# Optimization experiments

Measured on AMD Instinct MI355X. Metric: run time of the kernel, lower is better.

## Reference

```python
import jax, jax.numpy as jnp
import numpy as np

B, S, IN_F, OUT_F, GROUP = 2, 1024, 4096, 4096, 128
N_GROUPS = IN_F // GROUP  # 32


def setup_inputs() -> dict:
    key = jax.random.key(0)
    k1, k2, k3, k4 = jax.random.split(key, 4)
    x = jax.random.normal(k1, (B, S, IN_F), dtype=jnp.float32)
    # int4-range weights stored in int8, symmetric quant in [-7, 7]
    w_q = jax.random.randint(k2, (OUT_F, N_GROUPS, GROUP), -7, 8, dtype=jnp.int8)
    # per-(group, out_feature) scales, positive
    s_w = jax.random.uniform(k3, (N_GROUPS, OUT_F), dtype=jnp.float32,
                             minval=1e-3, maxval=2e-2)
    bias = jax.random.normal(k4, (OUT_F,), dtype=jnp.float32)
    return {"x": x, "w_q": w_q, "s_w": s_w, "bias": bias}


def reference(x, w_q, s_w, bias):
    # Faithful to QuantLinearW4Grouped.forward:
    #   y_g = einsum('ngk,ogk->ngo', x_f, w_f); y = (y_g * s_w[None]).sum(1) + bias
    # Expressed as a single fused einsum (identical math, no (n,g,o) intermediate).
    prefix = x.shape[:-1]
    orig_dtype = x.dtype
    xg = x.reshape(-1, N_GROUPS, GROUP).astype(jnp.float32)  # (n, g, k)
    w_f = w_q.astype(jnp.float32)                            # (o, g, k)
    y = jnp.einsum('ngk,ogk,go->no', xg, w_f, s_w)           # (n, o)
    y = y + bias.astype(y.dtype)
    return y.reshape(*prefix, OUT_F).astype(orig_dtype)
```

## Files before the change

### kernel.cpp

```cpp
#include <hip/hip_runtime.h>
#include <hip/hip_bf16.h>
#include <stdint.h>

#define M_TOK 2048
#define N_OUT 4096
#define K_IN  4096
#define GROUPSZ 128
#define NGRP  32

typedef signed char i8;
typedef int    intx4  __attribute__((ext_vector_type(4)));
typedef float  floatx4 __attribute__((ext_vector_type(4)));

#define XQ_BLOCKS (M_TOK)
#define WQ_BLOCKS (N_OUT * K_IN / 16 / 256)

__global__ __launch_bounds__(256) void quant_kernel(
    const float* __restrict__ x, const int* __restrict__ wq,
    i8* __restrict__ xq, i8* __restrict__ wq8, float* __restrict__ sx) {
  __shared__ float red[4];
  int b = blockIdx.x;
  int tid = threadIdx.x;
  if (b < XQ_BLOCKS) {
    const float* xr = x + (size_t)b * K_IN;
    int e0 = tid * 16;
    float4 v0 = *(const float4*)(xr + e0);
    float4 v1 = *(const float4*)(xr + e0 + 4);
    float4 v2 = *(const float4*)(xr + e0 + 8);
    float4 v3 = *(const float4*)(xr + e0 + 12);
    float m = fabsf(v0.x);
    m = fmaxf(m, fabsf(v0.y)); m = fmaxf(m, fabsf(v0.z)); m = fmaxf(m, fabsf(v0.w));
    m = fmaxf(m, fabsf(v1.x)); m = fmaxf(m, fabsf(v1.y)); m = fmaxf(m, fabsf(v1.z)); m = fmaxf(m, fabsf(v1.w));
    m = fmaxf(m, fabsf(v2.x)); m = fmaxf(m, fabsf(v2.y)); m = fmaxf(m, fabsf(v2.z)); m = fmaxf(m, fabsf(v2.w));
    m = fmaxf(m, fabsf(v3.x)); m = fmaxf(m, fabsf(v3.y)); m = fmaxf(m, fabsf(v3.z)); m = fmaxf(m, fabsf(v3.w));
#pragma unroll
    for (int off = 32; off > 0; off >>= 1)
      m = fmaxf(m, __shfl_xor(m, off, 64));
    int lane = tid & 63, wv = tid >> 6;
    if (lane == 0) red[wv] = m;
    __syncthreads();
    m = fmaxf(fmaxf(red[0], red[1]), fmaxf(red[2], red[3]));
    float inv = (m > 0.f) ? 127.f / m : 0.f;
    union { i8 q[16]; int4 v; } u;
    u.q[0]  = (i8)(int)rintf(v0.x * inv); u.q[1]  = (i8)(int)rintf(v0.y * inv);
    u.q[2]  = (i8)(int)rintf(v0.z * inv); u.q[3]  = (i8)(int)rintf(v0.w * inv);
    u.q[4]  = (i8)(int)rintf(v1.x * inv); u.q[5]  = (i8)(int)rintf(v1.y * inv);
    u.q[6]  = (i8)(int)rintf(v1.z * inv); u.q[7]  = (i8)(int)rintf(v1.w * inv);
    u.q[8]  = (i8)(int)rintf(v2.x * inv); u.q[9]  = (i8)(int)rintf(v2.y * inv);
    u.q[10] = (i8)(int)rintf(v2.z * inv); u.q[11] = (i8)(int)rintf(v2.w * inv);
    u.q[12] = (i8)(int)rintf(v3.x * inv); u.q[13] = (i8)(int)rintf(v3.y * inv);
    u.q[14] = (i8)(int)rintf(v3.z * inv); u.q[15] = (i8)(int)rintf(v3.w * inv);
    *(int4*)(xq + (size_t)b * K_IN + e0) = u.v;
    if (tid == 0) sx[b] = m * (1.f / 127.f);
  } else {
    size_t t = (size_t)(b - XQ_BLOCKS) * 256 + tid;
    size_t base = t * 16;
    const int* src = wq + base;
    int4 a0 = *(const int4*)(src);
    int4 a1 = *(const int4*)(src + 4);
    int4 a2 = *(const int4*)(src + 8);
    int4 a3 = *(const int4*)(src + 12);
    union { i8 q[16]; int4 v; } u;
    u.q[0]  = (i8)a0.x; u.q[1]  = (i8)a0.y; u.q[2]  = (i8)a0.z; u.q[3]  = (i8)a0.w;
    u.q[4]  = (i8)a1.x; u.q[5]  = (i8)a1.y; u.q[6]  = (i8)a1.z; u.q[7]  = (i8)a1.w;
    u.q[8]  = (i8)a2.x; u.q[9]  = (i8)a2.y; u.q[10] = (i8)a2.z; u.q[11] = (i8)a2.w;
    u.q[12] = (i8)a3.x; u.q[13] = (i8)a3.y; u.q[14] = (i8)a3.z; u.q[15] = (i8)a3.w;
    *(int4*)(wq8 + base) = u.v;
  }
}

#define BM 128
#define BN 128
#define BK 128

__global__ __launch_bounds__(256, 2) void gemm_i8_kernel(
    const i8* __restrict__ Aq, const i8* __restrict__ Bq,
    const float* __restrict__ sx, const float* __restrict__ sw,
    const float* __restrict__ bias, float* __restrict__ C) {
  __shared__ i8 As[BM * BK];
  __shared__ i8 Bs[BN * BK];
  __shared__ float sws[NGRP * BN];
  __shared__ float sxs[BM];

  const int tid  = threadIdx.x;
  const int lane = tid & 63;
  const int wave = tid >> 6;
  const int bm = blockIdx.y;
  const int bn = blockIdx.x;
  const int wm = wave >> 1;
  const int wn = wave & 1;

  const int rowA0 = bm * BM;
  const int rowB0 = bn * BN;

  {
    int g = tid >> 3, c0 = (tid & 7) * 16;
    const float* src = sw + (size_t)g * N_OUT + rowB0 + c0;
    float* dst = sws + g * BN + c0;
    *(float4*)(dst)      = *(const float4*)(src);
    *(float4*)(dst + 4)  = *(const float4*)(src + 4);
    *(float4*)(dst + 8)  = *(const float4*)(src + 8);
    *(float4*)(dst + 12) = *(const float4*)(src + 12);
    if (tid < BM) sxs[tid] = sx[rowA0 + tid];
  }

  const i8* srcA[4]; const i8* srcB[4];
#pragma unroll
  for (int i = 0; i < 4; ++i) {
    int chunk = i * 256 + tid;
    int row = chunk >> 3;
    int col = ((chunk & 7) ^ (row & 7)) << 4;
    srcA[i] = Aq + (size_t)(rowA0 + row) * K_IN + col;
    srcB[i] = Bq + (size_t)(rowB0 + row) * K_IN + col;
  }

  floatx4 master[4][4];
#pragma unroll
  for (int i = 0; i < 4; ++i)
#pragma unroll
    for (int j = 0; j < 4; ++j) master[i][j] = (floatx4)0.0f;

  const int quad = lane >> 4;
  const int l16  = lane & 15;
  const int h    = l16 & 7;
  const int x0   = (quad ^ h) * 16;
  const int x1   = x0 ^ 64;

  const intx4 MAGICV = {0x4B400000, 0x4B400000, 0x4B400000, 0x4B400000};
  const float MAGICF = 12582912.0f;

  for (int k0 = 0, g = 0; k0 < K_IN; k0 += BK, ++g) {
    __syncthreads();
#pragma unroll
    for (int i = 0; i < 4; ++i) {
      __builtin_amdgcn_global_load_lds(
          (const __attribute__((address_space(1))) void*)(srcA[i] + k0),
          (__attribute__((address_space(3))) void*)(As + (size_t)(i * 256 + wave * 64) * 16),
          16, 0, 0);
      __builtin_amdgcn_global_load_lds(
          (const __attribute__((address_space(1))) void*)(srcB[i] + k0),
          (__attribute__((address_space(3))) void*)(Bs + (size_t)(i * 256 + wave * 64) * 16),
          16, 0, 0);
    }
    __syncthreads();

    float swv[4];
#pragma unroll
    for (int j = 0; j < 4; ++j)
      swv[j] = sws[g * BN + wn * 64 + j * 16 + l16];

    intx4 a0[4], a1[4], b0[4], b1[4];
#pragma unroll
    for (int i = 0; i < 4; ++i) {
      const i8* pa = As + (size_t)(wm * 64 + i * 16 + l16) * BK;
      a0[i] = *(const intx4*)(pa + x0);
      a1[i] = *(const intx4*)(pa + x1);
    }
#pragma unroll
    for (int j = 0; j < 4; ++j) {
      const i8* pb = Bs + (size_t)(wn * 64 + j * 16 + l16) * BK;
      b0[j] = *(const intx4*)(pb + x0);
      b1[j] = *(const intx4*)(pb + x1);
    }

#pragma unroll
    for (int i = 0; i < 4; ++i)
#pragma unroll
      for (int j = 0; j < 4; ++j) {
        intx4 acc = __builtin_amdgcn_mfma_i32_16x16x64_i8(a0[i], b0[j], MAGICV, 0, 0, 0);
        acc = __builtin_amdgcn_mfma_i32_16x16x64_i8(a1[i], b1[j], acc, 0, 0, 0);
        floatx4 t = __builtin_bit_cast(floatx4, acc) - MAGICF;
        master[i][j] += t * swv[j];
      }
  }

#pragma unroll
  for (int j = 0; j < 4; ++j) {
    int col = rowB0 + wn * 64 + j * 16 + l16;
    float bv = bias[col];
#pragma unroll
    for (int i = 0; i < 4; ++i) {
      int rloc = wm * 64 + i * 16 + quad * 4;
#pragma unroll
      for (int r = 0; r < 4; ++r) {
        C[(size_t)(rowA0 + rloc + r) * N_OUT + col] =
            master[i][j][r] * sxs[rloc + r] + bv;
      }
    }
  }
}

extern "C" void kernel_launch(void* const* d_in, const int* in_sizes, int n_in,
                              void* d_out, int out_size, void* d_ws, size_t ws_size,
                              hipStream_t stream) {
  const float* x    = (const float*)d_in[0];
  const int*   wq   = (const int*)d_in[1];
  const float* sw   = (const float*)d_in[2];
  const float* bias = (const float*)d_in[3];
  float* out = (float*)d_out;

  i8*    xq  = (i8*)d_ws;
  i8*    wq8 = (i8*)((char*)d_ws + (size_t)M_TOK * K_IN);
  float* sx  = (float*)((char*)d_ws + (size_t)M_TOK * K_IN
                                     + (size_t)N_OUT * K_IN);

  {
    int nblocks = XQ_BLOCKS + WQ_BLOCKS;
    quant_kernel<<<nblocks, 256, 0, stream>>>(x, wq, xq, wq8, sx);
  }
  {
    dim3 grid(N_OUT / BN, M_TOK / BM);
    gemm_i8_kernel<<<grid, 256, 0, stream>>>(xq, wq8, sx, sw, bias, out);
  }
}
```

Measured before the change: 173.3 us.

## Double-buffer GEMM LDS tiles with 512-thread blocks and BK=64 prefetch pipeline

```diff
diff --git a/kernel.cpp b/kernel.cpp
--- a/kernel.cpp
+++ b/kernel.cpp
@@ -11,6 +11,9 @@
 typedef signed char i8;
 typedef int    intx4  __attribute__((ext_vector_type(4)));
 typedef float  floatx4 __attribute__((ext_vector_type(4)));
+
+#define AS1 __attribute__((address_space(1)))
+#define AS3 __attribute__((address_space(3)))
 
 #define XQ_BLOCKS (M_TOK)
 #define WQ_BLOCKS (N_OUT * K_IN / 16 / 256)
@@ -69,22 +72,24 @@
   }
 }
 
-#define BM 128
+#define BM 256
 #define BN 128
-#define BK 128
-
-__global__ __launch_bounds__(256, 2) void gemm_i8_kernel(
+#define BK 64
+#define NT (K_IN / BK)
+
+__global__ __launch_bounds__(512, 2) void gemm_i8_kernel(
     const i8* __restrict__ Aq, const i8* __restrict__ Bq,
     const float* __restrict__ sx, const float* __restrict__ sw,
     const float* __restrict__ bias, float* __restrict__ C) {
-  __shared__ i8 As[BM * BK];
-  __shared__ i8 Bs[BN * BK];
+  __shared__ i8 As[2 * BM * BK];
+  __shared__ i8 Bs[2 * BN * BK];
   __shared__ float sws[NGRP * BN];
-  __shared__ float sxs[BM];
 
   const int tid  = threadIdx.x;
   const int lane = tid & 63;
   const int wave = tid >> 6;
+  const int quad = lane >> 4;
+  const int l16  = lane & 15;
   const int bm = blockIdx.y;
   const int bn = blockIdx.x;
   const int wm = wave >> 1;
@@ -93,99 +98,101 @@
   const int rowA0 = bm * BM;
   const int rowB0 = bn * BN;
 
+  const int cA0 = tid, cA1 = 512 + tid, cB = tid;
+  const i8* srcA0 = Aq + (size_t)(rowA0 + (cA0 >> 2)) * K_IN
+                       + (((cA0 & 3) ^ ((cA0 >> 2) & 3)) << 4);
+  const i8* srcA1 = Aq + (size_t)(rowA0 + (cA1 >> 2)) * K_IN
+                       + (((cA1 & 3) ^ ((cA1 >> 2) & 3)) << 4);
+  const i8* srcB0 = Bq + (size_t)(rowB0 + (cB >> 2)) * K_IN
+                       + (((cB & 3) ^ ((cB >> 2) & 3)) << 4);
+  i8* dstA0 = As + (size_t)(wave * 64) * 16;
+  i8* dstA1 = As + (size_t)(512 + wave * 64) * 16;
+  i8* dstB0 = Bs + (size_t)(wave * 64) * 16;
+
+  auto stage = [&](int buf, int t) {
+    const size_t ko = (size_t)t * BK;
+    __builtin_amdgcn_global_load_lds(
+        (const AS1 void*)(srcA0 + ko),
+        (AS3 void*)(dstA0 + (size_t)buf * (BM * BK)), 16, 0, 0);
+    __builtin_amdgcn_global_load_lds(
+        (const AS1 void*)(srcA1 + ko),
+        (AS3 void*)(dstA1 + (size_t)buf * (BM * BK)), 16, 0, 0);
+    __builtin_amdgcn_global_load_lds(
+        (const AS1 void*)(srcB0 + ko),
+        (AS3 void*)(dstB0 + (size_t)buf * (BN * BK)), 16, 0, 0);
+  };
+
+  stage(0, 0);
   {
-    int g = tid >> 3, c0 = (tid & 7) * 16;
+    int g = tid >> 4, c0 = (tid & 15) * 8;
     const float* src = sw + (size_t)g * N_OUT + rowB0 + c0;
     float* dst = sws + g * BN + c0;
-    *(float4*)(dst)      = *(const float4*)(src);
-    *(float4*)(dst + 4)  = *(const float4*)(src + 4);
-    *(float4*)(dst + 8)  = *(const float4*)(src + 8);
-    *(float4*)(dst + 12) = *(const float4*)(src + 12);
-    if (tid < BM) sxs[tid] = sx[rowA0 + tid];
-  }
-
-  const i8* srcA[4]; const i8* srcB[4];
-#pragma unroll
-  for (int i = 0; i < 4; ++i) {
-    int chunk = i * 256 + tid;
-    int row = chunk >> 3;
-    int col = ((chunk & 7) ^ (row & 7)) << 4;
-    srcA[i] = Aq + (size_t)(rowA0 + row) * K_IN + col;
-    srcB[i] = Bq + (size_t)(rowB0 + row) * K_IN + col;
-  }
+    *(float4*)(dst)     = *(const float4*)(src);
+    *(float4*)(dst + 4) = *(const float4*)(src + 4);
+  }
+  __syncthreads();
 
   floatx4 master[4][4];
 #pragma unroll
   for (int i = 0; i < 4; ++i)
 #pragma unroll
     for (int j = 0; j < 4; ++j) master[i][j] = (floatx4)0.0f;
-
-  const int quad = lane >> 4;
-  const int l16  = lane & 15;
-  const int h    = l16 & 7;
-  const int x0   = (quad ^ h) * 16;
-  const int x1   = x0 ^ 64;
 
   const intx4 MAGICV = {0x4B400000, 0x4B400000, 0x4B400000, 0x4B400000};
   const float MAGICF = 12582912.0f;
 
-  for (int k0 = 0, g = 0; k0 < K_IN; k0 += BK, ++g) {
-    __syncthreads();
-#pragma unroll
-    for (int i = 0; i < 4; ++i) {
-      __builtin_amdgcn_global_load_lds(
-          (const __attribute__((address_space(1))) void*)(srcA[i] + k0),
-          (__attribute__((address_space(3))) void*)(As + (size_t)(i * 256 + wave * 64) * 16),
-          16, 0, 0);
-      __builtin_amdgcn_global_load_lds(
-          (const __attribute__((address_space(1))) void*)(srcB[i] + k0),
-          (__attribute__((address_space(3))) void*)(Bs + (size_t)(i * 256 + wave * 64) * 16),
-          16, 0, 0);
+  const int xk = (quad ^ (l16 & 3)) << 4;
+
+  for (int t = 0; t < NT; ++t) {
+    const int cur = t & 1;
+    if (t + 1 < NT) {
+      stage(cur ^ 1, t + 1);
+      asm volatile("s_waitcnt vmcnt(3)" ::: "memory");
+    } else {
+      asm volatile("s_waitcnt vmcnt(0)" ::: "memory");
     }
-    __syncthreads();
-
+    __builtin_amdgcn_s_barrier();
+
+    const i8* Ab = As + (size_t)cur * (BM * BK);
+    const i8* Bb = Bs + (size_t)cur * (BN * BK);
+    intx4 a[4], b[4];
+#pragma unroll
+    for (int i = 0; i < 4; ++i)
+      a[i] = *(const intx4*)(Ab + (size_t)(wm * 64 + i * 16 + l16) * BK + xk);
+#pragma unroll
+    for (int j = 0; j < 4; ++j)
+      b[j] = *(const intx4*)(Bb + (size_t)(wn * 64 + j * 16 + l16) * BK + xk);
+
+    const int g = t >> 1;
     float swv[4];
 #pragma unroll
     for (int j = 0; j < 4; ++j)
       swv[j] = sws[g * BN + wn * 64 + j * 16 + l16];
 
-    intx4 a0[4], a1[4], b0[4], b1[4];
-#pragma unroll
-    for (int i = 0; i < 4; ++i) {
-      const i8* pa = As + (size_t)(wm * 64 + i * 16 + l16) * BK;
-      a0[i] = *(const intx4*)(pa + x0);
-      a1[i] = *(const intx4*)(pa + x1);
-    }
+    asm volatile("s_waitcnt lgkmcnt(0)" ::: "memory");
+    __builtin_amdgcn_s_barrier();
+
+#pragma unroll
+    for (int i = 0; i < 4; ++i)
+#pragma unroll
+      for (int j = 0; j < 4; ++j) {
+        intx4 acc = __builtin_amdgcn_mfma_i32_16x16x64_i8(a[i], b[j], MAGICV, 0, 0, 0);
+        master[i][j] += (__builtin_bit_cast(floatx4, acc) - MAGICF) * swv[j];
+      }
+  }
+
+#pragma unroll
+  for (int i = 0; i < 4; ++i) {
+    float4 sxv = *(const float4*)(sx + rowA0 + wm * 64 + i * 16 + quad * 4);
 #pragma unroll
     for (int j = 0; j < 4; ++j) {
-      const i8* pb = Bs + (size_t)(wn * 64 + j * 16 + l16) * BK;
-      b0[j] = *(const intx4*)(pb + x0);
-      b1[j] = *(const intx4*)(pb + x1);
-    }
-
-#pragma unroll
-    for (int i = 0; i < 4; ++i)
-#pragma unroll
-      for (int j = 0; j < 4; ++j) {
-        intx4 acc = __builtin_amdgcn_mfma_i32_16x16x64_i8(a0[i], b0[j], MAGICV, 0, 0, 0);
-        acc = __builtin_amdgcn_mfma_i32_16x16x64_i8(a1[i], b1[j], acc, 0, 0, 0);
-        floatx4 t = __builtin_bit_cast(floatx4, acc) - MAGICF;
-        master[i][j] += t * swv[j];
-      }
-  }
-
-#pragma unroll
-  for (int j = 0; j < 4; ++j) {
-    int col = rowB0 + wn * 64 + j * 16 + l16;
-    float bv = bias[col];
-#pragma unroll
-    for (int i = 0; i < 4; ++i) {
+      int col = rowB0 + wn * 64 + j * 16 + l16;
+      float bv = bias[col];
       int rloc = wm * 64 + i * 16 + quad * 4;
-#pragma unroll
-      for (int r = 0; r < 4; ++r) {
-        C[(size_t)(rowA0 + rloc + r) * N_OUT + col] =
-            master[i][j][r] * sxs[rloc + r] + bv;
-      }
+      C[(size_t)(rowA0 + rloc + 0) * N_OUT + col] = master[i][j][0] * sxv.x + bv;
+      C[(size_t)(rowA0 + rloc + 1) * N_OUT + col] = master[i][j][1] * sxv.y + bv;
+      C[(size_t)(rowA0 + rloc + 2) * N_OUT + col] = master[i][j][2] * sxv.z + bv;
+      C[(size_t)(rowA0 + rloc + 3) * N_OUT + col] = master[i][j][3] * sxv.w + bv;
     }
   }
 }
@@ -210,6 +217,6 @@
   }
   {
     dim3 grid(N_OUT / BN, M_TOK / BM);
-    gemm_i8_kernel<<<grid, 256, 0, stream>>>(xq, wq8, sx, sw, bias, out);
+    gemm_i8_kernel<<<grid, 512, 0, stream>>>(xq, wq8, sx, sw, bias, out);
   }
 }
```

Result: slower. 202.1 us (+16.6%).
